# Kernel tuning notes

Hardware: AMD Instinct MI355X
Metric: run time of the kernel (lower is better)

## Reference

```python
import jax, jax.numpy as jnp
import numpy as np

B, L, D = 2, 2048, 2048
NUM_HEADS = 32
KV_GROUPS = 8
GROUP_SIZE = NUM_HEADS // KV_GROUPS  # 4
HEAD_DIM = D // NUM_HEADS            # 64


def _rope_tables(L, hd):
    # standard RoPE angle tables, duplicated across halves to width hd
    inv_freq = 1.0 / (10000.0 ** (np.arange(0, hd, 2, dtype=np.float32) / hd))
    ang = np.arange(L, dtype=np.float32)[:, None] * inv_freq[None, :]  # [L, hd/2]
    cos = np.concatenate([np.cos(ang), np.cos(ang)], axis=-1)
    sin = np.concatenate([np.sin(ang), np.sin(ang)], axis=-1)
    return jnp.asarray(cos), jnp.asarray(sin)


def setup_inputs() -> dict:
    key = jax.random.key(0)
    ks = jax.random.split(key, 6)
    x = jax.random.normal(ks[0], (B, L, D), dtype=jnp.float32)
    mask = jnp.triu(jnp.ones((L, L), dtype=bool), k=1)  # causal: True above diag
    cos, sin = _rope_tables(L, HEAD_DIM)
    s = 0.02
    Wq = jax.random.normal(ks[1], (D, D), dtype=jnp.float32) * s
    Wk = jax.random.normal(ks[2], (D, KV_GROUPS * HEAD_DIM), dtype=jnp.float32) * s
    Wv = jax.random.normal(ks[3], (D, KV_GROUPS * HEAD_DIM), dtype=jnp.float32) * s
    Wo = jax.random.normal(ks[4], (D, D), dtype=jnp.float32) * s
    bo = jnp.zeros((D,), dtype=jnp.float32)
    return {"x": x, "mask": mask, "cos": cos, "sin": sin,
            "Wq": Wq, "Wk": Wk, "Wv": Wv, "Wo": Wo, "bo": bo}


def _apply_rope(t, cos, sin):
    # t: [B, H, L, hd]
    hd = t.shape[-1]
    t1, t2 = t[..., : hd // 2], t[..., hd // 2:]
    rotated = jnp.concatenate([-t2, t1], axis=-1)
    return t * cos[None, None, :, :] + rotated * sin[None, None, :, :]


def reference(x, mask, cos, sin, Wq, Wk, Wv, Wo, bo):
    Bv, Lv, Dv = x.shape
    hd = HEAD_DIM
    q = (x @ Wq).reshape(Bv, Lv, NUM_HEADS, hd).transpose(0, 2, 1, 3)   # [B,H,L,hd]
    k = (x @ Wk).reshape(Bv, Lv, KV_GROUPS, hd).transpose(0, 2, 1, 3)   # [B,G,L,hd]
    v = (x @ Wv).reshape(Bv, Lv, KV_GROUPS, hd).transpose(0, 2, 1, 3)
    q = _apply_rope(q, cos, sin)
    k = _apply_rope(k, cos, sin)
    k = jnp.repeat(k, GROUP_SIZE, axis=1)  # [B,H,L,hd]
    v = jnp.repeat(v, GROUP_SIZE, axis=1)
    scores = jnp.einsum('bhqd,bhkd->bhqk', q, k) / jnp.sqrt(jnp.float32(hd))
    scores = jnp.where(mask[None, None, :, :], -jnp.inf, scores)
    attn = jax.nn.softmax(scores, axis=-1)
    out = jnp.einsum('bhqk,bhkd->bhqd', attn, v)         # [B,H,L,hd]
    out = out.transpose(0, 2, 1, 3).reshape(Bv, Lv, Dv)  # [B,L,D]
    return out @ Wo + bo
```

## Files before the change

kernel.cpp:

```cpp
#include <hip/hip_runtime.h>
#include <cstdint>

typedef unsigned short UST;
typedef __bf16 v8bf __attribute__((ext_vector_type(8)));
typedef float v4f __attribute__((ext_vector_type(4)));

static __device__ __forceinline__ UST f2b(float f) {
  union { float f; uint32_t u; } c; c.f = f;
  uint32_t u = c.u;
  u += 0x7fffu + ((u >> 16) & 1u);
  return (UST)(u >> 16);
}
static __device__ __forceinline__ float b2f(UST h) {
  union { uint32_t u; float f; } c; c.u = ((uint32_t)h) << 16;
  return c.f;
}
static __device__ __forceinline__ uint32_t cvtpk(float lo, float hi) {
  uint32_t r;
  asm("v_cvt_pk_bf16_f32 %0, %1, %2" : "=v"(r) : "v"(lo), "v"(hi));
  return r;
}
static __device__ __forceinline__ float fexp2(float x) {
  float r;
  asm("v_exp_f32 %0, %1" : "=v"(r) : "v"(x));
  return r;
}
template <int N>
static __device__ __forceinline__ void wait_vm() {
  asm volatile("s_waitcnt vmcnt(%0)" :: "i"(N));
}

static __device__ __forceinline__ void gl_lds16(const UST* g, UST* l) {
  __builtin_amdgcn_global_load_lds(
      (const __attribute__((address_space(1))) void*)g,
      (__attribute__((address_space(3))) void*)l, 16, 0, 0);
}

__global__ __launch_bounds__(256) void k_cast(const float* __restrict__ src,
                                              UST* __restrict__ dst) {
  size_t i = (size_t)blockIdx.x * 256 + threadIdx.x;
  const float4* s4 = reinterpret_cast<const float4*>(src) + 2 * i;
  float4 a = s4[0], b = s4[1];
  union { UST s[8]; uint4 v; } r;
  r.s[0] = f2b(a.x); r.s[1] = f2b(a.y); r.s[2] = f2b(a.z); r.s[3] = f2b(a.w);
  r.s[4] = f2b(b.x); r.s[5] = f2b(b.y); r.s[6] = f2b(b.z); r.s[7] = f2b(b.w);
  reinterpret_cast<uint4*>(dst)[i] = r.v;
}

__global__ __launch_bounds__(256) void k_castT(const float* __restrict__ W,
                                               UST* __restrict__ dst, int N, int K) {
  __shared__ float tile[32][33];
  int nt = blockIdx.x * 32, kt = blockIdx.y * 32;
  int tx = threadIdx.x, ty = threadIdx.y;
#pragma unroll
  for (int r = 0; r < 4; ++r)
    tile[ty + r * 8][tx] = W[(size_t)(kt + ty + r * 8) * N + nt + tx];
  __syncthreads();
#pragma unroll
  for (int r = 0; r < 4; ++r)
    dst[(size_t)(nt + ty + r * 8) * K + kt + tx] = f2b(tile[tx][ty + r * 8]);
}

template <int BM, int BN, int WM, int WN, int NMH, int EPI>
__global__ __launch_bounds__(512, 2) void k_gemm2(const UST* __restrict__ A,
                                                  const UST* __restrict__ Bt,
                                                  void* __restrict__ Cv,
                                                  const float* __restrict__ bias,
                                                  int M, int N, int K, int ntn) {
  constexpr int WMR = BM / WM, WNR = BN / WN;
  constexpr int MF = WMR / 16, NF = WNR / 16, MH = MF / NMH;
  constexpr int CA = BM / 128;
  constexpr int CBF = BN / 128;
  constexpr int BREM = (BN % 128) / 64;
  constexpr int AELEMS = 4 * BM * 32;
  __shared__ __align__(16) UST lds[AELEMS + 4 * BN * 32];

  int tid = threadIdx.x, w = tid >> 6, lane = tid & 63;
  int lr = lane & 15, lg = lane >> 4;
  int wm = w / WN, wn = w % WN;

  int q = (int)gridDim.x >> 3;
  int bid = (int)blockIdx.x;
  int swz = (bid & 7) * q + (bid >> 3);
  int mBlk = (swz / ntn) * BM, nBlk = (swz % ntn) * BN;

  v4f acc[MF][NF];
#pragma unroll
  for (int i = 0; i < MF; ++i)
#pragma unroll
    for (int j = 0; j < NF; ++j) acc[i][j] = (v4f){0.f, 0.f, 0.f, 0.f};

  int srow = tid >> 2;
  int scol = ((tid & 3) ^ ((tid >> 3) & 3)) * 8;
  const UST* Abase = A + (size_t)(mBlk + srow) * K + scol;
  const UST* Bbase = Bt + (size_t)(nBlk + srow) * K + scol;
  int ldsW = w * 512;

  auto stageA = [&](int buf, int s, int kt) {
#pragma unroll
    for (int i = 0; i < CA; ++i)
      gl_lds16(Abase + (size_t)(i * 128) * K + kt * 64 + s * 32,
               &lds[(buf * 2 + s) * BM * 32 + i * 4096 + ldsW]);
  };
  auto stageB = [&](int buf, int s, int kt) {
#pragma unroll
    for (int i = 0; i < CBF; ++i)
      gl_lds16(Bbase + (size_t)(i * 128) * K + kt * 64 + s * 32,
               &lds[AELEMS + (buf * 2 + s) * BN * 32 + i * 4096 + ldsW]);
    if constexpr (BREM) {
      if (w < 4)
        gl_lds16(Bbase + (size_t)(CBF * 128) * K + kt * 64 + s * 32,
                 &lds[AELEMS + (buf * 2 + s) * BN * 32 + CBF * 4096 + ldsW]);
    }
  };
  auto waitNK = [&]() {
    if constexpr (BREM) {
      if (w < 4) wait_vm<CA + CBF + 1>();
      else       wait_vm<CA + CBF>();
    } else {
      wait_vm<CA + CBF>();
    }
  };
  int rslot = ((lg ^ ((lr >> 1) & 3)) * 8);
  auto ldA = [&](int buf, int s, int f) -> v8bf {
    int row = wm * WMR + f * 16 + lr;
    return *(const v8bf*)&lds[((buf * 2 + s) * BM + row) * 32 + rslot];
  };
  auto ldB = [&](int buf, int s, int nf) -> v8bf {
    int row = wn * WNR + nf * 16 + lr;
    return *(const v8bf*)&lds[AELEMS + ((buf * 2 + s) * BN + row) * 32 + rslot];
  };

  int NT = K >> 6;
  stageA(0, 0, 0); stageB(0, 0, 0); stageA(0, 1, 0); stageB(0, 1, 0);
  waitNK();
  __builtin_amdgcn_s_barrier();

  for (int kt = 0; kt < NT; ++kt) {
    int buf = kt & 1, nb = buf ^ 1;
    bool more = (kt + 1 < NT);
#pragma unroll
    for (int s = 0; s < 2; ++s) {
      v8bf bfr[NF];
#pragma unroll
      for (int mh = 0; mh < NMH; ++mh) {
        v8bf afr[MH];
        if (mh == 0) {
#pragma unroll
          for (int nf = 0; nf < NF; ++nf) bfr[nf] = ldB(buf, s, nf);
        }
#pragma unroll
        for (int f = 0; f < MH; ++f) afr[f] = ldA(buf, s, mh * MH + f);
        if constexpr (NMH == 2) {
          if (mh == 0) {
            if (more) stageA(nb, s, kt + 1);
          } else {
            if (more) { stageB(nb, s, kt + 1); waitNK(); }
            else if (s == 0) wait_vm<0>();
          }
        } else {
          if (more) { stageA(nb, s, kt + 1); stageB(nb, s, kt + 1); waitNK(); }
          else if (s == 0) wait_vm<0>();
        }
        __builtin_amdgcn_s_barrier();
        __builtin_amdgcn_s_setprio(1);
#pragma unroll
        for (int f = 0; f < MH; ++f)
#pragma unroll
          for (int nf = 0; nf < NF; ++nf)
            acc[mh * MH + f][nf] = __builtin_amdgcn_mfma_f32_16x16x32_bf16(
                afr[f], bfr[nf], acc[mh * MH + f][nf], 0, 0, 0);
        __builtin_amdgcn_s_setprio(0);
        __builtin_amdgcn_s_barrier();
      }
    }
  }

  int row0 = mBlk + wm * WMR + lg * 4;
  int col0 = nBlk + wn * WNR + lr;
#pragma unroll
  for (int fm = 0; fm < MF; ++fm)
#pragma unroll
    for (int nf = 0; nf < NF; ++nf)
#pragma unroll
      for (int r = 0; r < 4; ++r) {
        int row = row0 + fm * 16 + r;
        int col = col0 + nf * 16;
        if constexpr (EPI == 0) {
          ((UST*)Cv)[(size_t)row * N + col] = f2b(acc[fm][nf][r]);
        } else {
          ((float*)Cv)[(size_t)row * N + col] = acc[fm][nf][r] + bias[col];
        }
      }
}

__global__ __launch_bounds__(256) void k_rope(const UST* __restrict__ qkv,
                                              const float* __restrict__ cosT,
                                              const float* __restrict__ sinT,
                                              UST* __restrict__ qh,
                                              UST* __restrict__ kh) {
  int idx = blockIdx.x * 256 + threadIdx.x;
  int q4 = idx & 3;
  int hh = (idx >> 2) % 40;
  int row = idx / 160;
  int l = row & 2047, b = row >> 11;
  int d0 = q4 * 8;
  int col = (hh < 32) ? hh * 64 : 2048 + (hh - 32) * 64;
  const UST* sp = qkv + (size_t)row * 3072 + col + d0;
  union { uint4 v; UST u[8]; } t1, t2, o1, o2;
  t1.v = *(const uint4*)sp;
  t2.v = *(const uint4*)(sp + 32);
  const float4* cp = (const float4*)&cosT[l * 64 + d0];
  const float4* sn = (const float4*)&sinT[l * 64 + d0];
  float4 ca = cp[0], cb = cp[1], sa = sn[0], sb = sn[1];
  float cc[8] = {ca.x, ca.y, ca.z, ca.w, cb.x, cb.y, cb.z, cb.w};
  float ss[8] = {sa.x, sa.y, sa.z, sa.w, sb.x, sb.y, sb.z, sb.w};
  float scale = (hh < 32) ? 0.125f : 1.f;
#pragma unroll
  for (int j = 0; j < 8; ++j) {
    float a = b2f(t1.u[j]), bb = b2f(t2.u[j]);
    o1.u[j] = f2b((a * cc[j] - bb * ss[j]) * scale);
    o2.u[j] = f2b((bb * cc[j] + a * ss[j]) * scale);
  }
  UST* dst = (hh < 32)
      ? qh + (((size_t)b * 32 + hh) * 2048 + l) * 64 + d0
      : kh + (((size_t)b * 8 + (hh - 32)) * 2048 + l) * 64 + d0;
  *(uint4*)dst = o1.v;
  *(uint4*)(dst + 32) = o2.v;
}

__global__ __launch_bounds__(256) void k_vtrans(const UST* __restrict__ qkv,
                                                UST* __restrict__ vt) {
  __shared__ __align__(16) UST tl[64][72];
  int lt = blockIdx.x, bg = blockIdx.y;
  int b = bg >> 3, g = bg & 7;
  int t = threadIdx.x;
  int li = t >> 2, d0 = (t & 3) * 16;
  const UST* src = qkv + (size_t)(b * 2048 + lt * 64 + li) * 3072 + 2560 + g * 64 + d0;
  *(uint4*)&tl[li][d0] = *(const uint4*)src;
  *(uint4*)&tl[li][d0 + 8] = *(const uint4*)(src + 8);
  __syncthreads();
  int d = t >> 2, l0 = (t & 3) * 16;
  union { UST u[8]; uint4 v; } r0, r1;
#pragma unroll
  for (int e = 0; e < 8; ++e) r0.u[e] = tl[l0 + e][d];
#pragma unroll
  for (int e = 0; e < 8; ++e) r1.u[e] = tl[l0 + 8 + e][d];
  UST* dstp = vt + (size_t)((b * 8 + g) * 64 + d) * 2048 + (size_t)lt * 64 + l0;
  *(uint4*)dstp = r0.v;
  *(uint4*)(dstp + 8) = r1.v;
}

__global__ __launch_bounds__(512, 4) void k_attn(const UST* __restrict__ qh,
                                                 const UST* __restrict__ kh,
                                                 const UST* __restrict__ vt,
                                                 UST* __restrict__ outp) {
  __shared__ __align__(16) UST k_s[128 * 72];
  __shared__ __align__(16) UST v_s[64 * 136];
  __shared__ __align__(16) UST p_s[8][16 * 136];
  int bx = blockIdx.x, h = blockIdx.y, b = blockIdx.z;
  int g = h >> 2;
  int tid = threadIdx.x, w = tid >> 6, lane = tid & 63;
  int lr = lane & 15, lg = lane >> 4;

  int ksr = tid >> 2, ksc = (tid & 3) * 16;
  int vsr = tid >> 3, vsc = (tid & 7) * 16;
  const UST* kbase = kh + ((size_t)(b * 8 + g) * 2048 + ksr) * 64 + ksc;
  const UST* vbase = vt + ((size_t)(b * 8 + g) * 64 + vsr) * 2048 + vsc;
  UST* kdst = &k_s[ksr * 72 + ksc];
  UST* vdst = &v_s[vsr * 136 + vsc];

  for (int half = 0; half < 2; ++half) {
    int qt = half ? (15 - bx) : bx;
    int qbase = qt * 128 + w * 16;

    const UST* qp = qh + ((size_t)(b * 32 + h) * 2048 + qbase + lr) * 64 + lg * 8;
    v8bf qf0 = *(const v8bf*)qp;
    v8bf qf1 = *(const v8bf*)(qp + 32);

    float m = -1e30f, ls = 0.f;
    v4f o[4];
#pragma unroll
    for (int dt = 0; dt < 4; ++dt) o[dt] = (v4f){0.f, 0.f, 0.f, 0.f};

    __syncthreads();
    uint4 pk0 = *(const uint4*)kbase, pk1 = *(const uint4*)(kbase + 8);
    uint4 pv0 = *(const uint4*)vbase, pv1 = *(const uint4*)(vbase + 8);
    *(uint4*)kdst = pk0; *(uint4*)(kdst + 8) = pk1;
    *(uint4*)vdst = pv0; *(uint4*)(vdst + 8) = pv1;

    for (int j = 0; j <= qt; ++j) {
      __syncthreads();
      bool pref = (j < qt);
      if (pref) {
        const UST* kg = kbase + (size_t)(j + 1) * 8192;
        const UST* vg = vbase + (j + 1) * 128;
        pk0 = *(const uint4*)kg; pk1 = *(const uint4*)(kg + 8);
        pv0 = *(const uint4*)vg; pv1 = *(const uint4*)(vg + 8);
      }

      v4f st[8];
      __builtin_amdgcn_s_setprio(1);
#pragma unroll
      for (int kt = 0; kt < 8; ++kt) {
        const UST* kr = &k_s[(kt * 16 + lr) * 72 + lg * 8];
        v8bf kf0 = *(const v8bf*)kr;
        v8bf kf1 = *(const v8bf*)(kr + 32);
        v4f z = (v4f){0.f, 0.f, 0.f, 0.f};
        z = __builtin_amdgcn_mfma_f32_16x16x32_bf16(kf0, qf0, z, 0, 0, 0);
        z = __builtin_amdgcn_mfma_f32_16x16x32_bf16(kf1, qf1, z, 0, 0, 0);
        st[kt] = z;
      }
      __builtin_amdgcn_s_setprio(0);
      if (j == qt) {
        int qg = qbase + lr;
#pragma unroll
        for (int kt = 0; kt < 8; ++kt)
#pragma unroll
          for (int r = 0; r < 4; ++r) {
            int kg2 = j * 128 + kt * 16 + 4 * lg + r;
            if (kg2 > qg) st[kt][r] = -1e30f;
          }
      }

      float t0 = fmaxf(fmaxf(st[0][0], st[0][1]), fmaxf(st[0][2], st[0][3]));
      float t1 = fmaxf(fmaxf(st[1][0], st[1][1]), fmaxf(st[1][2], st[1][3]));
      float t2 = fmaxf(fmaxf(st[2][0], st[2][1]), fmaxf(st[2][2], st[2][3]));
      float t3 = fmaxf(fmaxf(st[3][0], st[3][1]), fmaxf(st[3][2], st[3][3]));
      float t4 = fmaxf(fmaxf(st[4][0], st[4][1]), fmaxf(st[4][2], st[4][3]));
      float t5 = fmaxf(fmaxf(st[5][0], st[5][1]), fmaxf(st[5][2], st[5][3]));
      float t6 = fmaxf(fmaxf(st[6][0], st[6][1]), fmaxf(st[6][2], st[6][3]));
      float t7 = fmaxf(fmaxf(st[7][0], st[7][1]), fmaxf(st[7][2], st[7][3]));
      float mx = fmaxf(fmaxf(fmaxf(t0, t1), fmaxf(t2, t3)),
                       fmaxf(fmaxf(t4, t5), fmaxf(t6, t7)));
      mx = fmaxf(mx, __shfl_xor(mx, 16));
      mx = fmaxf(mx, __shfl_xor(mx, 32));

      if (!__all(mx <= m + 8.f)) {
        float mn = fmaxf(m, mx);
        float al = __expf(m - mn);
        m = mn;
        ls *= al;
#pragma unroll
        for (int r = 0; r < 4; ++r) {
          float ar = __shfl(al, 4 * lg + r);
          o[0][r] *= ar; o[1][r] *= ar; o[2][r] *= ar; o[3][r] *= ar;
        }
      }

      constexpr float LOG2E = 1.44269504f;
      float mlog = m * LOG2E;
      float rs = 0.f;
      UST* pw = &p_s[w][lr * 136 + 4 * lg];
#pragma unroll
      for (int kt = 0; kt < 8; ++kt) {
        float p0 = fexp2(__builtin_fmaf(st[kt][0], LOG2E, -mlog));
        float p1 = fexp2(__builtin_fmaf(st[kt][1], LOG2E, -mlog));
        float p2 = fexp2(__builtin_fmaf(st[kt][2], LOG2E, -mlog));
        float p3 = fexp2(__builtin_fmaf(st[kt][3], LOG2E, -mlog));
        rs += (p0 + p1) + (p2 + p3);
        uint2 q2;
        q2.x = cvtpk(p0, p1);
        q2.y = cvtpk(p2, p3);
        *(uint2*)(pw + kt * 16) = q2;
      }

      __builtin_amdgcn_s_setprio(1);
#pragma unroll
      for (int kk = 0; kk < 4; ++kk) {
        v8bf pa = *(const v8bf*)&p_s[w][lr * 136 + kk * 32 + lg * 8];
#pragma unroll
        for (int dt = 0; dt < 4; ++dt) {
          v8bf vb = *(const v8bf*)&v_s[(dt * 16 + lr) * 136 + kk * 32 + lg * 8];
          o[dt] = __builtin_amdgcn_mfma_f32_16x16x32_bf16(pa, vb, o[dt], 0, 0, 0);
        }
      }
      __builtin_amdgcn_s_setprio(0);

      rs += __shfl_xor(rs, 16);
      rs += __shfl_xor(rs, 32);
      ls += rs;

      __syncthreads();
      if (pref) {
        *(uint4*)kdst = pk0; *(uint4*)(kdst + 8) = pk1;
        *(uint4*)vdst = pv0; *(uint4*)(vdst + 8) = pv1;
      }
    }

    float iv = 1.f / ls;
#pragma unroll
    for (int r = 0; r < 4; ++r) {
      float ivr = __shfl(iv, 4 * lg + r);
      size_t rowb = ((size_t)b * 2048 + qbase + 4 * lg + r) * 2048 + h * 64 + lr;
#pragma unroll
      for (int dt = 0; dt < 4; ++dt)
        outp[rowb + dt * 16] = f2b(o[dt][r] * ivr);
    }
  }
}

extern "C" void kernel_launch(void* const* d_in, const int* in_sizes, int n_in,
                              void* d_out, int out_size, void* d_ws, size_t ws_size,
                              hipStream_t stream) {
  const float* x    = (const float*)d_in[0];
  const float* cosT = (const float*)d_in[2];
  const float* sinT = (const float*)d_in[3];
  const float* Wq   = (const float*)d_in[4];
  const float* Wk   = (const float*)d_in[5];
  const float* Wv   = (const float*)d_in[6];
  const float* Wo   = (const float*)d_in[7];
  const float* bo   = (const float*)d_in[8];
  float* out = (float*)d_out;

  char* ws = (char*)d_ws;
  UST* xb   = (UST*)(ws);
  UST* wcat = (UST*)(ws + 16777216);
  UST* wot  = (UST*)(ws + 29360128);
  UST* qkv  = (UST*)(ws + 37748736);
  UST* qhp  = (UST*)(ws + 62914560);
  UST* khp  = (UST*)(ws + 79691776);
  UST* vtp  = (UST*)(ws + 83886080);
  UST* attn_o = xb;

  k_cast<<<4096, 256, 0, stream>>>(x, xb);
  k_castT<<<dim3(64, 64), dim3(32, 8), 0, stream>>>(Wq, wcat, 2048, 2048);
  k_castT<<<dim3(16, 64), dim3(32, 8), 0, stream>>>(Wk, wcat + (size_t)2048 * 2048, 512, 2048);
  k_castT<<<dim3(16, 64), dim3(32, 8), 0, stream>>>(Wv, wcat + (size_t)2560 * 2048, 512, 2048);
  k_castT<<<dim3(64, 64), dim3(32, 8), 0, stream>>>(Wo, wot, 2048, 2048);

  k_gemm2<256, 192, 2, 4, 2, 0><<<256, 512, 0, stream>>>(xb, wcat, qkv, nullptr,
                                                         4096, 3072, 2048, 16);
  k_rope<<<2560, 256, 0, stream>>>(qkv, cosT, sinT, qhp, khp);
  k_vtrans<<<dim3(32, 16), 256, 0, stream>>>(qkv, vtp);
  k_attn<<<dim3(8, 32, 2), 512, 0, stream>>>(qhp, khp, vtp, attn_o);
  k_gemm2<256, 128, 4, 2, 1, 1><<<256, 512, 0, stream>>>(attn_o, wot, out, bo,
                                                         4096, 2048, 2048, 16);
}
```

Measured before the change: 201.4 us.

## Replace double-buffered GEMM K loop with 4-slot ring prefetching three slices ahead

The GEMM main loop changes from double buffering of 64-wide K tiles (two 32-wide halves each) to a 4-slot ring of 32-wide K slices. Loads are issued three slices ahead, and the wait allows two slices of loads to stay in flight. The aim is to hide more global-to-LDS latency behind MFMA work and to smooth out when load instructions are issued. The LDS footprint stays the same, since it is still four slices, but the vmcnt counts are larger, and the stageSlice k-offset formula deserves a close check.

Result: faster. 197.4 us (-2.0%).

```diff
diff --git a/kernel.cpp b/kernel.cpp
--- a/kernel.cpp
+++ b/kernel.cpp
@@ -96,85 +96,80 @@
   const UST* Bbase = Bt + (size_t)(nBlk + srow) * K + scol;
   int ldsW = w * 512;
 
-  auto stageA = [&](int buf, int s, int kt) {
+  auto stageSlice = [&](int v) {
+    int reg = v & 3;
+    int koff = (v >> 1) * 64 + (v & 1) * 32;
 #pragma unroll
     for (int i = 0; i < CA; ++i)
-      gl_lds16(Abase + (size_t)(i * 128) * K + kt * 64 + s * 32,
-               &lds[(buf * 2 + s) * BM * 32 + i * 4096 + ldsW]);
-  };
-  auto stageB = [&](int buf, int s, int kt) {
+      gl_lds16(Abase + (size_t)(i * 128) * K + koff,
+               &lds[reg * BM * 32 + i * 4096 + ldsW]);
 #pragma unroll
     for (int i = 0; i < CBF; ++i)
-      gl_lds16(Bbase + (size_t)(i * 128) * K + kt * 64 + s * 32,
-               &lds[AELEMS + (buf * 2 + s) * BN * 32 + i * 4096 + ldsW]);
+      gl_lds16(Bbase + (size_t)(i * 128) * K + koff,
+               &lds[AELEMS + reg * BN * 32 + i * 4096 + ldsW]);
     if constexpr (BREM) {
       if (w < 4)
-        gl_lds16(Bbase + (size_t)(CBF * 128) * K + kt * 64 + s * 32,
-                 &lds[AELEMS + (buf * 2 + s) * BN * 32 + CBF * 4096 + ldsW]);
+        gl_lds16(Bbase + (size_t)(CBF * 128) * K + koff,
+                 &lds[AELEMS + reg * BN * 32 + CBF * 4096 + ldsW]);
     }
   };
-  auto waitNK = [&]() {
+  auto wait2 = [&]() {
     if constexpr (BREM) {
-      if (w < 4) wait_vm<CA + CBF + 1>();
-      else       wait_vm<CA + CBF>();
+      if (w < 4) wait_vm<2 * (CA + CBF + 1)>();
+      else       wait_vm<2 * (CA + CBF)>();
     } else {
-      wait_vm<CA + CBF>();
+      wait_vm<2 * (CA + CBF)>();
     }
   };
   int rslot = ((lg ^ ((lr >> 1) & 3)) * 8);
-  auto ldA = [&](int buf, int s, int f) -> v8bf {
+  auto ldA = [&](int reg, int f) -> v8bf {
     int row = wm * WMR + f * 16 + lr;
-    return *(const v8bf*)&lds[((buf * 2 + s) * BM + row) * 32 + rslot];
+    return *(const v8bf*)&lds[(reg * BM + row) * 32 + rslot];
   };
-  auto ldB = [&](int buf, int s, int nf) -> v8bf {
+  auto ldB = [&](int reg, int nf) -> v8bf {
     int row = wn * WNR + nf * 16 + lr;
-    return *(const v8bf*)&lds[AELEMS + ((buf * 2 + s) * BN + row) * 32 + rslot];
+    return *(const v8bf*)&lds[AELEMS + (reg * BN + row) * 32 + rslot];
   };
 
-  int NT = K >> 6;
-  stageA(0, 0, 0); stageB(0, 0, 0); stageA(0, 1, 0); stageB(0, 1, 0);
-  waitNK();
+  int U = K >> 5;
+  stageSlice(0); stageSlice(1); stageSlice(2);
+  wait2();
   __builtin_amdgcn_s_barrier();
 
-  for (int kt = 0; kt < NT; ++kt) {
-    int buf = kt & 1, nb = buf ^ 1;
-    bool more = (kt + 1 < NT);
-#pragma unroll
-    for (int s = 0; s < 2; ++s) {
-      v8bf bfr[NF];
-#pragma unroll
-      for (int mh = 0; mh < NMH; ++mh) {
-        v8bf afr[MH];
-        if (mh == 0) {
-#pragma unroll
-          for (int nf = 0; nf < NF; ++nf) bfr[nf] = ldB(buf, s, nf);
-        }
-#pragma unroll
-        for (int f = 0; f < MH; ++f) afr[f] = ldA(buf, s, mh * MH + f);
-        if constexpr (NMH == 2) {
-          if (mh == 0) {
-            if (more) stageA(nb, s, kt + 1);
-          } else {
-            if (more) { stageB(nb, s, kt + 1); waitNK(); }
-            else if (s == 0) wait_vm<0>();
-          }
-        } else {
-          if (more) { stageA(nb, s, kt + 1); stageB(nb, s, kt + 1); waitNK(); }
-          else if (s == 0) wait_vm<0>();
-        }
-        __builtin_amdgcn_s_barrier();
-        __builtin_amdgcn_s_setprio(1);
-#pragma unroll
-        for (int f = 0; f < MH; ++f)
-#pragma unroll
-          for (int nf = 0; nf < NF; ++nf)
-            acc[mh * MH + f][nf] = __builtin_amdgcn_mfma_f32_16x16x32_bf16(
-                afr[f], bfr[nf], acc[mh * MH + f][nf], 0, 0, 0);
-        __builtin_amdgcn_s_setprio(0);
-        __builtin_amdgcn_s_barrier();
-      }
+  auto slice = [&](int u, bool issue, int wkind) {
+    int reg = u & 3;
+    v8bf bfr[NF];
+#pragma unroll
+    for (int mh = 0; mh < NMH; ++mh) {
+      v8bf afr[MH];
+      if (mh == 0) {
+#pragma unroll
+        for (int nf = 0; nf < NF; ++nf) bfr[nf] = ldB(reg, nf);
+      }
+#pragma unroll
+      for (int f = 0; f < MH; ++f) afr[f] = ldA(reg, mh * MH + f);
+      if (mh == 0 && issue) stageSlice(u + 3);
+      if (mh == NMH - 1) {
+        if (wkind == 1) wait2();
+        else if (wkind == 2) wait_vm<0>();
+      }
+      __builtin_amdgcn_s_barrier();
+      __builtin_amdgcn_s_setprio(1);
+#pragma unroll
+      for (int f = 0; f < MH; ++f)
+#pragma unroll
+        for (int nf = 0; nf < NF; ++nf)
+          acc[mh * MH + f][nf] = __builtin_amdgcn_mfma_f32_16x16x32_bf16(
+              afr[f], bfr[nf], acc[mh * MH + f][nf], 0, 0, 0);
+      __builtin_amdgcn_s_setprio(0);
+      __builtin_amdgcn_s_barrier();
     }
-  }
+  };
+
+  for (int u = 0; u < U - 3; ++u) slice(u, true, 1);
+  slice(U - 3, false, 2);
+  slice(U - 2, false, 0);
+  slice(U - 1, false, 0);
 
   int row0 = mBlk + wm * WMR + lg * 4;
   int col0 = nBlk + wn * WNR + lr;
```
